# Kernel tuning notes

Measured on AMD Instinct MI355X. Metric: run time of the kernel, lower is better.

Reference implementation:

```python
import jax, jax.numpy as jnp
import numpy as np

C = 512        # channels
CTX = 768      # context_dim


def setup_inputs() -> dict:
    key = jax.random.key(0)
    ks = jax.random.split(key, 10)
    B, H, W = 8, 64, 64
    Lc = 512
    s = 0.02
    return {
        "x": jax.random.normal(ks[0], (B, C, H, W), jnp.float32),
        "context": jax.random.normal(ks[1], (B, Lc, CTX), jnp.float32),
        "Wq": jax.random.normal(ks[2], (C, C), jnp.float32) * s,
        "bq": jnp.zeros((C,), jnp.float32),
        "Wk": jax.random.normal(ks[3], (CTX, C), jnp.float32) * s,
        "bk": jnp.zeros((C,), jnp.float32),
        "Wv": jax.random.normal(ks[4], (CTX, C), jnp.float32) * s,
        "bv": jnp.zeros((C,), jnp.float32),
        "Wo": jax.random.normal(ks[5], (C, C), jnp.float32) * s,
        "bo": jnp.zeros((C,), jnp.float32),
    }


def reference(x, context, Wq, bq, Wk, bk, Wv, bv, Wo, bo):
    B, Cdim, H, W = x.shape
    scale = Cdim ** (-0.5)
    # [B, HW, C]
    xr = x.reshape(B, Cdim, H * W).transpose(0, 2, 1)
    q = xr @ Wq + bq                      # [B, HW, C]
    k = context @ Wk + bk                 # [B, Lc, C]
    v = context @ Wv + bv                 # [B, Lc, C]
    sim = jnp.einsum('bqc,bkc->bqk', q, k) * scale
    attn = jax.nn.softmax(sim, axis=-1)
    out = jnp.einsum('bqk,bkc->bqc', attn, v)
    out = out @ Wo + bo                   # [B, HW, C]
    out = out.transpose(0, 2, 1).reshape(B, Cdim, H, W)
    return x + out
```

## Files before the change

kernel.cpp:

```cpp
#include <hip/hip_runtime.h>
#include <hip/hip_bf16.h>

typedef __bf16 bf16_t;
typedef bf16_t bf16x8 __attribute__((ext_vector_type(8)));
typedef bf16_t bf16x4 __attribute__((ext_vector_type(4)));
typedef float  f32x4  __attribute__((ext_vector_type(4)));

constexpr int B_ = 8, C_ = 512, HW_ = 4096, LC_ = 512, CTX_ = 768;


__global__ void k_transpose_w(const float* __restrict__ in, bf16_t* __restrict__ out,
                              int R, int Cc) {
    __shared__ float t[32][33];
    int r0 = blockIdx.x * 32, c0 = blockIdx.y * 32;
    int tx = threadIdx.x, ty = threadIdx.y;
#pragma unroll
    for (int i = 0; i < 4; ++i)
        t[ty + i * 8][tx] = in[(size_t)(r0 + ty + i * 8) * Cc + c0 + tx];
    __syncthreads();
#pragma unroll
    for (int i = 0; i < 4; ++i)
        out[(size_t)(c0 + ty + i * 8) * R + r0 + tx] = (bf16_t)t[tx][ty + i * 8];
}

__global__ void k_bias(const float* __restrict__ bk, const float* __restrict__ bv,
                       const bf16_t* __restrict__ Wo_t, const float* __restrict__ bo,
                       float* __restrict__ bkvo) {
    int blk = blockIdx.x, tid = threadIdx.x;
    if (blk >= 128) {
        int i = (blk - 128) * 256 + tid;
        bkvo[i] = bk[i];
        return;
    }
    int wave = tid >> 6, lane = tid & 63;
    int cc = blk * 4 + wave;
    bf16x8 w = *(const bf16x8*)&Wo_t[(size_t)cc * C_ + lane * 8];
    float s = 0.f;
#pragma unroll
    for (int j = 0; j < 8; ++j) s += bv[lane * 8 + j] * (float)w[j];
#pragma unroll
    for (int o = 32; o > 0; o >>= 1) s += __shfl_xor(s, o);
    if (lane == 0) bkvo[512 + cc] = s + bo[cc];
}

__global__ void k_f32_to_bf16(const float* __restrict__ in, bf16_t* __restrict__ out, int n) {
    int i = (blockIdx.x * 256 + threadIdx.x) * 4;
    if (i >= n) return;
    f32x4 v = *(const f32x4*)(in + i);
    bf16x4 w;
    w[0] = (bf16_t)v.x; w[1] = (bf16_t)v.y; w[2] = (bf16_t)v.z; w[3] = (bf16_t)v.w;
    *(bf16x4*)(out + i) = w;
}

template <int MODE>
__global__ __launch_bounds__(256) void k_gemm(
    const bf16_t* __restrict__ A, int lda, long sA,
    const bf16_t* __restrict__ Bt, int ldb, long sB,
    const float* __restrict__ bias,
    void* __restrict__ out_, long sOut,
    int N, int K, float scale) {
    __shared__ bf16_t lA[128 * 32];
    __shared__ bf16_t lB[128 * 32];
    const int z = blockIdx.z;
    A  += (size_t)z * sA;
    Bt += (size_t)z * sB;
    const int tid  = threadIdx.x;
    const int lane = tid & 63;
    const int wave = tid >> 6;
    const int wm = (wave >> 1) * 64, wn = (wave & 1) * 64;
    const int bm0 = blockIdx.y * 128, bn0 = blockIdx.x * 128;
    const int ar = lane & 15, kc = lane >> 4;

    auto lA3 = (__attribute__((address_space(3))) char*)&lA[0];
    auto lB3 = (__attribute__((address_space(3))) char*)&lB[0];

    f32x4 acc[4][4] = {};

    for (int k0 = 0; k0 < K; k0 += 32) {
        __syncthreads();
#pragma unroll
        for (int s = 0; s < 2; ++s) {
            int wchunk = wave * 2 + s;
            int id = wchunk * 64 + lane;
            int row = id >> 2, c4 = id & 3;
            __builtin_amdgcn_global_load_lds(
                (const __attribute__((address_space(1))) void*)
                    &A[(size_t)(bm0 + row) * lda + k0 + c4 * 8],
                (__attribute__((address_space(3))) void*)(lA3 + wchunk * 1024),
                16, 0, 0);
            __builtin_amdgcn_global_load_lds(
                (const __attribute__((address_space(1))) void*)
                    &Bt[(size_t)(bn0 + row) * ldb + k0 + c4 * 8],
                (__attribute__((address_space(3))) void*)(lB3 + wchunk * 1024),
                16, 0, 0);
        }
        __syncthreads();
        bf16x8 af[4], bfr[4];
#pragma unroll
        for (int f = 0; f < 4; ++f) {
            af[f]  = *(const bf16x8*)&lA[(wm + f * 16 + ar) * 32 + kc * 8];
            bfr[f] = *(const bf16x8*)&lB[(wn + f * 16 + ar) * 32 + kc * 8];
        }
#pragma unroll
        for (int fm = 0; fm < 4; ++fm)
#pragma unroll
            for (int fn = 0; fn < 4; ++fn)
                acc[fm][fn] = __builtin_amdgcn_mfma_f32_16x16x32_bf16(
                    af[fm], bfr[fn], acc[fm][fn], 0, 0, 0);
    }

    const int rj = (lane >> 4) * 4;
    const int cj = lane & 15;

#pragma unroll
    for (int fm = 0; fm < 4; ++fm) {
#pragma unroll
        for (int fn = 0; fn < 4; ++fn) {
            int r0 = bm0 + wm + fm * 16 + rj;
            int cc = bn0 + wn + fn * 16 + cj;
            if constexpr (MODE == 3) {
                bf16_t* out = (bf16_t*)out_;
                bf16x4 v;
#pragma unroll
                for (int j = 0; j < 4; ++j) v[j] = (bf16_t)acc[fm][fn][j];
                *(bf16x4*)&out[(size_t)cc * sOut + r0] = v;
            } else {
                float bb = bias[cc];
                if (cc < 512) {
                    bf16_t* o = (bf16_t*)out_;
#pragma unroll
                    for (int j = 0; j < 4; ++j)
                        o[(size_t)(r0 + j) * 512 + cc] = (bf16_t)(acc[fm][fn][j] + bb);
                } else {
                    bf16_t* o = (bf16_t*)out_ + (size_t)B_ * LC_ * C_;
                    int b = r0 >> 9, l0 = r0 & 511;
                    bf16x4 v;
#pragma unroll
                    for (int j = 0; j < 4; ++j) v[j] = (bf16_t)(acc[fm][fn][j] + bb);
                    *(bf16x4*)&o[((size_t)b * C_ + (cc - 512)) * LC_ + l0] = v;
                }
            }
        }
    }
}

__global__ __launch_bounds__(512, 2) void k_flash(
    const bf16_t* __restrict__ Wq_t, const float* __restrict__ bq,
    const bf16_t* __restrict__ Kb, const bf16_t* __restrict__ Vt,
    const float* __restrict__ x, float* __restrict__ out) {
    __shared__ bf16_t lQP[64 * 512];
    __shared__ bf16_t lS[3][16384];
    float (*redA)[64] = (float(*)[64])&lQP[0];
    float (*redB)[64] = (float(*)[64])&lQP[512];

    const int bid = blockIdx.x;
    const int z = bid & 7;
    const int q0 = (bid >> 3) * 64;
    const int tid = threadIdx.x;
    const int lane = tid & 63;
    const int wave = tid >> 6;
    const int wm2 = wave >> 2;
    const int wn4 = wave & 3;
    const int h = lane >> 4;
    const int r15 = lane & 15;

    const bf16_t* Kz = Kb + (size_t)z * LC_ * C_;
    const bf16_t* Vz = Vt + (size_t)z * C_ * LC_;
    const float*  xz = x + (size_t)z * C_ * HW_;

    auto lS3 = (__attribute__((address_space(3))) char*)&lS[0][0];

    auto STAGE = [&](int b, const bf16_t* __restrict__ src, int t) {
#pragma unroll
        for (int s = 0; s < 4; ++s) {
            int id = s * 512 + tid;
            int row = id >> 2, c4 = id & 3;
            int c4s = c4 ^ (row & 3);
            __builtin_amdgcn_global_load_lds(
                (const __attribute__((address_space(1))) void*)
                    &src[(size_t)row * 512 + t * 32 + c4s * 8],
                (__attribute__((address_space(3))) void*)
                    (lS3 + b * 32768 + s * 8192 + wave * 1024),
                16, 0, 0);
        }
    };

    f32x4 acc[2][8];
    bf16x8 af0[2], bf0[8], af1[2], bf1[8];

    auto READF = [&](bf16x8 (&af)[2], bf16x8 (&bfr)[8], int t, int buf) {
        int c16 = t * 4 + h;
#pragma unroll
        for (int m = 0; m < 2; ++m) {
            int row = wm2 * 32 + m * 16 + r15;
            int sc = (c16 & 56) | ((c16 ^ row) & 7);
            af[m] = *(const bf16x8*)&lQP[row * 512 + sc * 8];
        }
        const bf16_t* lb = &lS[buf][0];
#pragma unroll
        for (int n = 0; n < 8; ++n) {
            int row = wn4 * 128 + n * 16 + r15;
            bfr[n] = *(const bf16x8*)&lb[row * 32 + (h ^ (row & 3)) * 8];
        }
    };
    auto MF = [&](bf16x8 (&af)[2], bf16x8 (&bfr)[8]) {
        __builtin_amdgcn_s_setprio(1);
#pragma unroll
        for (int m = 0; m < 2; ++m)
#pragma unroll
            for (int n = 0; n < 8; ++n)
                acc[m][n] = __builtin_amdgcn_mfma_f32_16x16x32_bf16(
                    af[m], bfr[n], acc[m][n], 0, 0, 0);
        __builtin_amdgcn_s_setprio(0);
    };
    auto BAR = [&]() {
        __builtin_amdgcn_sched_barrier(0);
        __builtin_amdgcn_s_barrier();
        __builtin_amdgcn_sched_barrier(0);
    };

    auto PHASE = [&](const bf16_t* __restrict__ src, int off) {
        READF(af0, bf0, 0, off % 3);
#pragma unroll
        for (int tt = 0; tt < 7; ++tt) {
            int t = 2 * tt;
            STAGE((t + 2 + off) % 3, src, t + 2);
            MF(af0, bf0);
            asm volatile("s_waitcnt vmcnt(4)" ::: "memory");
            READF(af1, bf1, t + 1, (t + 1 + off) % 3);
            BAR();
            STAGE((t + 3 + off) % 3, src, t + 3);
            MF(af1, bf1);
            asm volatile("s_waitcnt vmcnt(4)" ::: "memory");
            READF(af0, bf0, t + 2, (t + 2 + off) % 3);
            BAR();
        }
        MF(af0, bf0);
        asm volatile("s_waitcnt vmcnt(0)" ::: "memory");
        READF(af1, bf1, 15, (15 + off) % 3);
        BAR();
        MF(af1, bf1);
    };

    STAGE(0, Wq_t, 0); STAGE(1, Wq_t, 1);
#pragma unroll
    for (int i = 0; i < 16; ++i) {
        int c = i * 32 + (tid >> 4);
        int q = (tid & 15) * 4;
        f32x4 v = *(const f32x4*)&xz[(size_t)c * HW_ + q0 + q];
#pragma unroll
        for (int j = 0; j < 4; ++j) {
            int row = q + j;
            int c16 = c >> 3;
            int sc = (c16 & 56) | ((c16 ^ row) & 7);
            lQP[row * 512 + sc * 8 + (c & 7)] = (bf16_t)v[j];
        }
    }
    __syncthreads();

#pragma unroll
    for (int m = 0; m < 2; ++m)
#pragma unroll
        for (int n = 0; n < 8; ++n) acc[m][n] = (f32x4)0.f;
    PHASE(Wq_t, 0);

    __syncthreads();
    STAGE(1, Kz, 0); STAGE(2, Kz, 1);
    {
        float bqv[8];
#pragma unroll
        for (int n = 0; n < 8; ++n) bqv[n] = bq[wn4 * 128 + n * 16 + r15];
#pragma unroll
        for (int m = 0; m < 2; ++m)
#pragma unroll
            for (int j = 0; j < 4; ++j) {
                int row = wm2 * 32 + m * 16 + h * 4 + j;
#pragma unroll
                for (int n = 0; n < 8; ++n) {
                    int col = wn4 * 128 + n * 16 + r15;
                    int c16 = col >> 3;
                    int sc = (c16 & 56) | ((c16 ^ row) & 7);
                    lQP[row * 512 + sc * 8 + (col & 7)] = (bf16_t)(acc[m][n][j] + bqv[n]);
                }
            }
    }
    __syncthreads();

#pragma unroll
    for (int m = 0; m < 2; ++m)
#pragma unroll
        for (int n = 0; n < 8; ++n) acc[m][n] = (f32x4)0.f;
    PHASE(Kz, 1);

    __syncthreads();
    STAGE(2, Vz, 0); STAGE(0, Vz, 1);
    const float scale = 0.044194173824159216f;
    float M[2][4], inv[2][4];
#pragma unroll
    for (int m = 0; m < 2; ++m)
#pragma unroll
        for (int j = 0; j < 4; ++j) {
            float v = -1e30f;
#pragma unroll
            for (int n = 0; n < 8; ++n) v = fmaxf(v, acc[m][n][j]);
#pragma unroll
            for (int o = 1; o < 16; o <<= 1) v = fmaxf(v, __shfl_xor(v, o));
            if (r15 == 0) redA[wn4][wm2 * 32 + m * 16 + h * 4 + j] = v;
        }
    __syncthreads();
#pragma unroll
    for (int m = 0; m < 2; ++m)
#pragma unroll
        for (int j = 0; j < 4; ++j) {
            int row = wm2 * 32 + m * 16 + h * 4 + j;
            M[m][j] = fmaxf(fmaxf(redA[0][row], redA[1][row]),
                            fmaxf(redA[2][row], redA[3][row]));
        }
#pragma unroll
    for (int m = 0; m < 2; ++m)
#pragma unroll
        for (int j = 0; j < 4; ++j) {
            float s = 0.f;
#pragma unroll
            for (int n = 0; n < 8; ++n) {
                float e = __expf((acc[m][n][j] - M[m][j]) * scale);
                acc[m][n][j] = e;
                s += e;
            }
#pragma unroll
            for (int o = 1; o < 16; o <<= 1) s += __shfl_xor(s, o);
            if (r15 == 0) redB[wn4][wm2 * 32 + m * 16 + h * 4 + j] = s;
        }
    __syncthreads();
#pragma unroll
    for (int m = 0; m < 2; ++m)
#pragma unroll
        for (int j = 0; j < 4; ++j) {
            int row = wm2 * 32 + m * 16 + h * 4 + j;
            inv[m][j] = 1.f / (redB[0][row] + redB[1][row] +
                               redB[2][row] + redB[3][row]);
        }
    __syncthreads();
#pragma unroll
    for (int m = 0; m < 2; ++m)
#pragma unroll
        for (int j = 0; j < 4; ++j) {
            int row = wm2 * 32 + m * 16 + h * 4 + j;
#pragma unroll
            for (int n = 0; n < 8; ++n) {
                int col = wn4 * 128 + n * 16 + r15;
                int c16 = col >> 3;
                int sc = (c16 & 56) | ((c16 ^ row) & 7);
                lQP[row * 512 + sc * 8 + (col & 7)] = (bf16_t)(acc[m][n][j] * inv[m][j]);
            }
        }
    __syncthreads();

#pragma unroll
    for (int m = 0; m < 2; ++m)
#pragma unroll
        for (int n = 0; n < 8; ++n) acc[m][n] = (f32x4)0.f;
    PHASE(Vz, 2);

    float* oz = out + (size_t)z * C_ * HW_;
#pragma unroll
    for (int m = 0; m < 2; ++m)
#pragma unroll
        for (int n = 0; n < 8; ++n) {
            int r0 = q0 + wm2 * 32 + m * 16 + h * 4;
            int cc = wn4 * 128 + n * 16 + r15;
            f32x4 xv = *(const f32x4*)&xz[(size_t)cc * HW_ + r0];
            f32x4 o;
#pragma unroll
            for (int j = 0; j < 4; ++j) o[j] = acc[m][n][j] + xv[j];
            *(f32x4*)&oz[(size_t)cc * HW_ + r0] = o;
        }
}

extern "C" void kernel_launch(void* const* d_in, const int* in_sizes, int n_in,
                              void* d_out, int out_size, void* d_ws, size_t ws_size,
                              hipStream_t stream) {
    (void)in_sizes; (void)n_in; (void)out_size; (void)ws_size;
    const float* x   = (const float*)d_in[0];
    const float* ctx = (const float*)d_in[1];
    const float* Wq  = (const float*)d_in[2];
    const float* bq  = (const float*)d_in[3];
    const float* Wk  = (const float*)d_in[4];
    const float* bk  = (const float*)d_in[5];
    const float* Wv  = (const float*)d_in[6];
    const float* bv  = (const float*)d_in[7];
    const float* Wo  = (const float*)d_in[8];
    const float* bo  = (const float*)d_in[9];
    float* out = (float*)d_out;

    char* ws = (char*)d_ws;
    size_t off = 0;
    auto alloc = [&](size_t bytes) {
        char* p = ws + off;
        off += (bytes + 255) & ~(size_t)255;
        return p;
    };
    bf16_t* Wq_t  = (bf16_t*)alloc((size_t)C_ * C_ * 2);
    bf16_t* Wk_t  = (bf16_t*)alloc((size_t)C_ * CTX_ * 2);
    bf16_t* Wvo_t = (bf16_t*)alloc((size_t)C_ * CTX_ * 2);
    bf16_t* Wv_b  = (bf16_t*)alloc((size_t)CTX_ * C_ * 2);
    bf16_t* Wo_t  = (bf16_t*)alloc((size_t)C_ * C_ * 2);
    float*  bkvo  = (float*)alloc((size_t)1024 * 4);
    bf16_t* ctxb  = (bf16_t*)alloc((size_t)B_ * LC_ * CTX_ * 2);
    bf16_t* Kb    = (bf16_t*)alloc((size_t)B_ * LC_ * C_ * 2);
    bf16_t* Vt    = (bf16_t*)alloc((size_t)B_ * C_ * LC_ * 2);

    k_transpose_w<<<dim3(C_ / 32, C_ / 32), dim3(32, 8), 0, stream>>>(Wq, Wq_t, C_, C_);
    k_transpose_w<<<dim3(CTX_ / 32, C_ / 32), dim3(32, 8), 0, stream>>>(Wk, Wk_t, CTX_, C_);
    k_transpose_w<<<dim3(C_ / 32, C_ / 32), dim3(32, 8), 0, stream>>>(Wo, Wo_t, C_, C_);
    k_f32_to_bf16<<<(CTX_ * C_ / 4 + 255) / 256, 256, 0, stream>>>(Wv, Wv_b, CTX_ * C_);
    k_bias<<<130, 256, 0, stream>>>(bk, bv, Wo_t, bo, bkvo);
    k_f32_to_bf16<<<(B_ * LC_ * CTX_ / 4 + 255) / 256, 256, 0, stream>>>(
        ctx, ctxb, B_ * LC_ * CTX_);

    k_gemm<3><<<dim3(4, 6, 1), 256, 0, stream>>>(
        Wv_b, C_, 0, Wo_t, C_, 0, nullptr, Wvo_t, CTX_, C_, C_, 1.f);
    k_gemm<4><<<dim3(8, 32, 1), 256, 0, stream>>>(
        ctxb, CTX_, 0, Wk_t, CTX_, 0, bkvo, Kb, 0, 1024, CTX_, 1.f);
    k_flash<<<512, 512, 0, stream>>>(Wq_t, bq, Kb, Vt, x, out);
}
```

Before: 165.6 us.

## Re-tile flash kernel waves as 1x8 with 64x64 tiles and merge weight transposes

Each wave in the fused attention kernel now covers all 64 query rows and 64 output columns (a 4x4 MFMA tile) instead of 32 rows by 128 columns. This changes the ratio of A to B fragment loads, and the K-loop becomes a simple single-buffered-register loop with one barrier per step. The LDS swizzle for staged tiles switches to row>>1 to match the new read pattern. Softmax reductions now combine 8 waves instead of 4, so the redB scratch offset moves to avoid overlapping redA. The three weight-transpose launches are merged into one 3D-grid launch to cut launch overhead. In exchange, there is less register-level software pipelining of LDS reads against the MFMAs.

```diff
diff --git a/kernel.cpp b/kernel.cpp
--- a/kernel.cpp
+++ b/kernel.cpp
@@ -9,14 +9,21 @@
 constexpr int B_ = 8, C_ = 512, HW_ = 4096, LC_ = 512, CTX_ = 768;
 
 
-__global__ void k_transpose_w(const float* __restrict__ in, bf16_t* __restrict__ out,
-                              int R, int Cc) {
+__global__ void k_transpose_w3(const float* __restrict__ Wq, const float* __restrict__ Wk,
+                               const float* __restrict__ Wo,
+                               bf16_t* __restrict__ Wq_t, bf16_t* __restrict__ Wk_t,
+                               bf16_t* __restrict__ Wo_t) {
     __shared__ float t[32][33];
+    int zz = blockIdx.z;
+    const float* in = (zz == 0) ? Wq : (zz == 1) ? Wk : Wo;
+    bf16_t* out     = (zz == 0) ? Wq_t : (zz == 1) ? Wk_t : Wo_t;
+    int R = (zz == 1) ? CTX_ : C_;
     int r0 = blockIdx.x * 32, c0 = blockIdx.y * 32;
+    if (r0 >= R) return;
     int tx = threadIdx.x, ty = threadIdx.y;
 #pragma unroll
     for (int i = 0; i < 4; ++i)
-        t[ty + i * 8][tx] = in[(size_t)(r0 + ty + i * 8) * Cc + c0 + tx];
+        t[ty + i * 8][tx] = in[(size_t)(r0 + ty + i * 8) * C_ + c0 + tx];
     __syncthreads();
 #pragma unroll
     for (int i = 0; i < 4; ++i)
@@ -151,7 +158,7 @@
     __shared__ bf16_t lQP[64 * 512];
     __shared__ bf16_t lS[3][16384];
     float (*redA)[64] = (float(*)[64])&lQP[0];
-    float (*redB)[64] = (float(*)[64])&lQP[512];
+    float (*redB)[64] = (float(*)[64])&lQP[1024];
 
     const int bid = blockIdx.x;
     const int z = bid & 7;
@@ -159,8 +166,6 @@
     const int tid = threadIdx.x;
     const int lane = tid & 63;
     const int wave = tid >> 6;
-    const int wm2 = wave >> 2;
-    const int wn4 = wave & 3;
     const int h = lane >> 4;
     const int r15 = lane & 15;
 
@@ -175,7 +180,7 @@
         for (int s = 0; s < 4; ++s) {
             int id = s * 512 + tid;
             int row = id >> 2, c4 = id & 3;
-            int c4s = c4 ^ (row & 3);
+            int c4s = c4 ^ ((row >> 1) & 3);
             __builtin_amdgcn_global_load_lds(
                 (const __attribute__((address_space(1))) void*)
                     &src[(size_t)row * 512 + t * 32 + c4s * 8],
@@ -185,61 +190,41 @@
         }
     };
 
-    f32x4 acc[2][8];
-    bf16x8 af0[2], bf0[8], af1[2], bf1[8];
-
-    auto READF = [&](bf16x8 (&af)[2], bf16x8 (&bfr)[8], int t, int buf) {
-        int c16 = t * 4 + h;
-#pragma unroll
-        for (int m = 0; m < 2; ++m) {
-            int row = wm2 * 32 + m * 16 + r15;
-            int sc = (c16 & 56) | ((c16 ^ row) & 7);
-            af[m] = *(const bf16x8*)&lQP[row * 512 + sc * 8];
-        }
-        const bf16_t* lb = &lS[buf][0];
-#pragma unroll
-        for (int n = 0; n < 8; ++n) {
-            int row = wn4 * 128 + n * 16 + r15;
-            bfr[n] = *(const bf16x8*)&lb[row * 32 + (h ^ (row & 3)) * 8];
-        }
-    };
-    auto MF = [&](bf16x8 (&af)[2], bf16x8 (&bfr)[8]) {
-        __builtin_amdgcn_s_setprio(1);
-#pragma unroll
-        for (int m = 0; m < 2; ++m)
-#pragma unroll
-            for (int n = 0; n < 8; ++n)
-                acc[m][n] = __builtin_amdgcn_mfma_f32_16x16x32_bf16(
-                    af[m], bfr[n], acc[m][n], 0, 0, 0);
-        __builtin_amdgcn_s_setprio(0);
-    };
-    auto BAR = [&]() {
-        __builtin_amdgcn_sched_barrier(0);
-        __builtin_amdgcn_s_barrier();
-        __builtin_amdgcn_sched_barrier(0);
-    };
+    f32x4 acc[4][4];
 
     auto PHASE = [&](const bf16_t* __restrict__ src, int off) {
-        READF(af0, bf0, 0, off % 3);
-#pragma unroll
-        for (int tt = 0; tt < 7; ++tt) {
-            int t = 2 * tt;
-            STAGE((t + 2 + off) % 3, src, t + 2);
-            MF(af0, bf0);
-            asm volatile("s_waitcnt vmcnt(4)" ::: "memory");
-            READF(af1, bf1, t + 1, (t + 1 + off) % 3);
-            BAR();
-            STAGE((t + 3 + off) % 3, src, t + 3);
-            MF(af1, bf1);
-            asm volatile("s_waitcnt vmcnt(4)" ::: "memory");
-            READF(af0, bf0, t + 2, (t + 2 + off) % 3);
-            BAR();
-        }
-        MF(af0, bf0);
-        asm volatile("s_waitcnt vmcnt(0)" ::: "memory");
-        READF(af1, bf1, 15, (15 + off) % 3);
-        BAR();
-        MF(af1, bf1);
+        for (int t = 0; t < 16; ++t) {
+            if (t <= 13) STAGE((t + 2 + off) % 3, src, t + 2);
+            bf16x8 af[4], bfr[4];
+            int c16 = t * 4 + h;
+#pragma unroll
+            for (int m = 0; m < 4; ++m) {
+                int row = m * 16 + r15;
+                int sc = (c16 & 56) | ((c16 ^ row) & 7);
+                af[m] = *(const bf16x8*)&lQP[row * 512 + sc * 8];
+            }
+            const bf16_t* lb = &lS[(t + off) % 3][0];
+#pragma unroll
+            for (int n = 0; n < 4; ++n) {
+                int row = wave * 64 + n * 16 + r15;
+                bfr[n] = *(const bf16x8*)&lb[row * 32 + ((h ^ (row >> 1)) & 3) * 8];
+            }
+            __builtin_amdgcn_s_setprio(1);
+#pragma unroll
+            for (int m = 0; m < 4; ++m)
+#pragma unroll
+                for (int n = 0; n < 4; ++n)
+                    acc[m][n] = __builtin_amdgcn_mfma_f32_16x16x32_bf16(
+                        af[m], bfr[n], acc[m][n], 0, 0, 0);
+            __builtin_amdgcn_s_setprio(0);
+            if (t < 15) {
+                if (t <= 13) asm volatile("s_waitcnt vmcnt(4)" ::: "memory");
+                else         asm volatile("s_waitcnt vmcnt(0)" ::: "memory");
+                __builtin_amdgcn_sched_barrier(0);
+                __builtin_amdgcn_s_barrier();
+                __builtin_amdgcn_sched_barrier(0);
+            }
+        }
     };
 
     STAGE(0, Wq_t, 0); STAGE(1, Wq_t, 1);
@@ -259,25 +244,25 @@
     __syncthreads();
 
 #pragma unroll
-    for (int m = 0; m < 2; ++m)
-#pragma unroll
-        for (int n = 0; n < 8; ++n) acc[m][n] = (f32x4)0.f;
+    for (int m = 0; m < 4; ++m)
+#pragma unroll
+        for (int n = 0; n < 4; ++n) acc[m][n] = (f32x4)0.f;
     PHASE(Wq_t, 0);
 
     __syncthreads();
     STAGE(1, Kz, 0); STAGE(2, Kz, 1);
     {
-        float bqv[8];
-#pragma unroll
-        for (int n = 0; n < 8; ++n) bqv[n] = bq[wn4 * 128 + n * 16 + r15];
-#pragma unroll
-        for (int m = 0; m < 2; ++m)
+        float bqv[4];
+#pragma unroll
+        for (int n = 0; n < 4; ++n) bqv[n] = bq[wave * 64 + n * 16 + r15];
+#pragma unroll
+        for (int m = 0; m < 4; ++m)
 #pragma unroll
             for (int j = 0; j < 4; ++j) {
-                int row = wm2 * 32 + m * 16 + h * 4 + j;
-#pragma unroll
-                for (int n = 0; n < 8; ++n) {
-                    int col = wn4 * 128 + n * 16 + r15;
+                int row = m * 16 + h * 4 + j;
+#pragma unroll
+                for (int n = 0; n < 4; ++n) {
+                    int col = wave * 64 + n * 16 + r15;
                     int c16 = col >> 3;
                     int sc = (c16 & 56) | ((c16 ^ row) & 7);
                     lQP[row * 512 + sc * 8 + (col & 7)] = (bf16_t)(acc[m][n][j] + bqv[n]);
@@ -287,68 +272,71 @@
     __syncthreads();
 
 #pragma unroll
-    for (int m = 0; m < 2; ++m)
-#pragma unroll
-        for (int n = 0; n < 8; ++n) acc[m][n] = (f32x4)0.f;
+    for (int m = 0; m < 4; ++m)
+#pragma unroll
+        for (int n = 0; n < 4; ++n) acc[m][n] = (f32x4)0.f;
     PHASE(Kz, 1);
 
     __syncthreads();
     STAGE(2, Vz, 0); STAGE(0, Vz, 1);
     const float scale = 0.044194173824159216f;
-    float M[2][4], inv[2][4];
-#pragma unroll
-    for (int m = 0; m < 2; ++m)
-#pragma unroll
-        for (int j = 0; j < 4; ++j) {
-            float v = -1e30f;
-#pragma unroll
-            for (int n = 0; n < 8; ++n) v = fmaxf(v, acc[m][n][j]);
+    float M[4][4], inv[4][4];
+#pragma unroll
+    for (int m = 0; m < 4; ++m)
+#pragma unroll
+        for (int j = 0; j < 4; ++j) {
+            float v = fmaxf(fmaxf(acc[m][0][j], acc[m][1][j]),
+                            fmaxf(acc[m][2][j], acc[m][3][j]));
 #pragma unroll
             for (int o = 1; o < 16; o <<= 1) v = fmaxf(v, __shfl_xor(v, o));
-            if (r15 == 0) redA[wn4][wm2 * 32 + m * 16 + h * 4 + j] = v;
-        }
-    __syncthreads();
-#pragma unroll
-    for (int m = 0; m < 2; ++m)
-#pragma unroll
-        for (int j = 0; j < 4; ++j) {
-            int row = wm2 * 32 + m * 16 + h * 4 + j;
-            M[m][j] = fmaxf(fmaxf(redA[0][row], redA[1][row]),
-                            fmaxf(redA[2][row], redA[3][row]));
-        }
-#pragma unroll
-    for (int m = 0; m < 2; ++m)
+            if (r15 == 0) redA[wave][m * 16 + h * 4 + j] = v;
+        }
+    __syncthreads();
+#pragma unroll
+    for (int m = 0; m < 4; ++m)
+#pragma unroll
+        for (int j = 0; j < 4; ++j) {
+            int row = m * 16 + h * 4 + j;
+            float v = redA[0][row];
+#pragma unroll
+            for (int w = 1; w < 8; ++w) v = fmaxf(v, redA[w][row]);
+            M[m][j] = v;
+        }
+#pragma unroll
+    for (int m = 0; m < 4; ++m)
 #pragma unroll
         for (int j = 0; j < 4; ++j) {
             float s = 0.f;
 #pragma unroll
-            for (int n = 0; n < 8; ++n) {
+            for (int n = 0; n < 4; ++n) {
                 float e = __expf((acc[m][n][j] - M[m][j]) * scale);
                 acc[m][n][j] = e;
                 s += e;
             }
 #pragma unroll
             for (int o = 1; o < 16; o <<= 1) s += __shfl_xor(s, o);
-            if (r15 == 0) redB[wn4][wm2 * 32 + m * 16 + h * 4 + j] = s;
-        }
-    __syncthreads();
-#pragma unroll
-    for (int m = 0; m < 2; ++m)
-#pragma unroll
-        for (int j = 0; j < 4; ++j) {
-            int row = wm2 * 32 + m * 16 + h * 4 + j;
-            inv[m][j] = 1.f / (redB[0][row] + redB[1][row] +
-                               redB[2][row] + redB[3][row]);
-        }
-    __syncthreads();
-#pragma unroll
-    for (int m = 0; m < 2; ++m)
-#pragma unroll
-        for (int j = 0; j < 4; ++j) {
-            int row = wm2 * 32 + m * 16 + h * 4 + j;
-#pragma unroll
-            for (int n = 0; n < 8; ++n) {
-                int col = wn4 * 128 + n * 16 + r15;
+            if (r15 == 0) redB[wave][m * 16 + h * 4 + j] = s;
+        }
+    __syncthreads();
+#pragma unroll
+    for (int m = 0; m < 4; ++m)
+#pragma unroll
+        for (int j = 0; j < 4; ++j) {
+            int row = m * 16 + h * 4 + j;
+            float s = redB[0][row];
+#pragma unroll
+            for (int w = 1; w < 8; ++w) s += redB[w][row];
+            inv[m][j] = 1.f / s;
+        }
+    __syncthreads();
+#pragma unroll
+    for (int m = 0; m < 4; ++m)
+#pragma unroll
+        for (int j = 0; j < 4; ++j) {
+            int row = m * 16 + h * 4 + j;
+#pragma unroll
+            for (int n = 0; n < 4; ++n) {
+                int col = wave * 64 + n * 16 + r15;
                 int c16 = col >> 3;
                 int sc = (c16 & 56) | ((c16 ^ row) & 7);
                 lQP[row * 512 + sc * 8 + (col & 7)] = (bf16_t)(acc[m][n][j] * inv[m][j]);
@@ -357,18 +345,18 @@
     __syncthreads();
 
 #pragma unroll
-    for (int m = 0; m < 2; ++m)
-#pragma unroll
-        for (int n = 0; n < 8; ++n) acc[m][n] = (f32x4)0.f;
+    for (int m = 0; m < 4; ++m)
+#pragma unroll
+        for (int n = 0; n < 4; ++n) acc[m][n] = (f32x4)0.f;
     PHASE(Vz, 2);
 
     float* oz = out + (size_t)z * C_ * HW_;
 #pragma unroll
-    for (int m = 0; m < 2; ++m)
-#pragma unroll
-        for (int n = 0; n < 8; ++n) {
-            int r0 = q0 + wm2 * 32 + m * 16 + h * 4;
-            int cc = wn4 * 128 + n * 16 + r15;
+    for (int m = 0; m < 4; ++m)
+#pragma unroll
+        for (int n = 0; n < 4; ++n) {
+            int r0 = q0 + m * 16 + h * 4;
+            int cc = wave * 64 + n * 16 + r15;
             f32x4 xv = *(const f32x4*)&xz[(size_t)cc * HW_ + r0];
             f32x4 o;
 #pragma unroll
@@ -410,9 +398,8 @@
     bf16_t* Kb    = (bf16_t*)alloc((size_t)B_ * LC_ * C_ * 2);
     bf16_t* Vt    = (bf16_t*)alloc((size_t)B_ * C_ * LC_ * 2);
 
-    k_transpose_w<<<dim3(C_ / 32, C_ / 32), dim3(32, 8), 0, stream>>>(Wq, Wq_t, C_, C_);
-    k_transpose_w<<<dim3(CTX_ / 32, C_ / 32), dim3(32, 8), 0, stream>>>(Wk, Wk_t, CTX_, C_);
-    k_transpose_w<<<dim3(C_ / 32, C_ / 32), dim3(32, 8), 0, stream>>>(Wo, Wo_t, C_, C_);
+    k_transpose_w3<<<dim3(CTX_ / 32, C_ / 32, 3), dim3(32, 8), 0, stream>>>(
+        Wq, Wk, Wo, Wq_t, Wk_t, Wo_t);
     k_f32_to_bf16<<<(CTX_ * C_ / 4 + 255) / 256, 256, 0, stream>>>(Wv, Wv_b, CTX_ * C_);
     k_bias<<<130, 256, 0, stream>>>(bk, bv, Wo_t, bo, bkvo);
     k_f32_to_bf16<<<(B_ * LC_ * CTX_ / 4 + 255) / 256, 256, 0, stream>>>(
```

New measurement: 185.5 us. 12.0% more time.
